# Performance work log

Measured on AMD Instinct MI355X. Metric: run time of the kernel, lower is better.

The kernel has to match this reference:

```python
import jax, jax.numpy as jnp
import numpy as np

HIDDEN = 2048
N_HEADS = 16
HEAD_DIM = HIDDEN // N_HEADS
ROPE_THETA = 10000.0
BSZ, SEQ = 2, 2048
NEG_INF = -1e9


def setup_inputs() -> dict:
    key = jax.random.key(0)
    ks = jax.random.split(key, 5)
    scale = 1.0 / np.sqrt(HIDDEN)
    hidden_states = jax.random.normal(ks[0], (BSZ, SEQ, HIDDEN), dtype=jnp.float32)
    Wq = jax.random.normal(ks[1], (HIDDEN, HIDDEN), dtype=jnp.float32) * scale
    Wk = jax.random.normal(ks[2], (HIDDEN, HIDDEN), dtype=jnp.float32) * scale
    Wv = jax.random.normal(ks[3], (HIDDEN, HIDDEN), dtype=jnp.float32) * scale
    Wo = jax.random.normal(ks[4], (HIDDEN, HIDDEN), dtype=jnp.float32) * scale
    # additive causal mask, [1, 1, S, S]
    causal = jnp.triu(jnp.full((SEQ, SEQ), NEG_INF, dtype=jnp.float32), k=1)
    attention_mask = causal[None, None, :, :]
    position_ids = jnp.arange(SEQ, dtype=jnp.int32)
    return {
        "hidden_states": hidden_states,
        "Wq": Wq, "Wk": Wk, "Wv": Wv, "Wo": Wo,
        "attention_mask": attention_mask,
        "position_ids": position_ids,
    }


def _rotate_half(x):
    half = x.shape[-1] // 2
    return jnp.concatenate((-x[..., half:], x[..., :half]), axis=-1)


def _rope_tables(seq_len, position_ids):
    # inv_freq: [head_dim/2]
    inv_freq = 1.0 / (ROPE_THETA ** (jnp.arange(0, HEAD_DIM, 2, dtype=jnp.float32) / HEAD_DIM))
    t = jnp.arange(seq_len, dtype=jnp.float32)
    freqs = t[:, None] * inv_freq[None, :]              # [S, D/2]
    emb = jnp.concatenate((freqs, freqs), axis=-1)      # [S, D]
    cos = jnp.cos(emb)[position_ids]                    # [S, D]
    sin = jnp.sin(emb)[position_ids]
    return cos, sin


def reference(hidden_states, Wq, Wk, Wv, Wo, attention_mask, position_ids):
    b, s, h = hidden_states.shape
    def proj(W):
        return (hidden_states @ W.T).reshape(b, s, N_HEADS, HEAD_DIM).transpose(0, 2, 1, 3)
    q = proj(Wq)  # [B, H, S, D]
    k = proj(Wk)
    v = proj(Wv)
    cos, sin = _rope_tables(s, position_ids)            # [S, D], broadcasts over B,H
    q = q * cos + _rotate_half(q) * sin
    k = k * cos + _rotate_half(k) * sin
    scores = jnp.einsum('bhqd,bhkd->bhqk', q, k) / np.sqrt(HEAD_DIM)
    scores = scores + attention_mask
    w = jax.nn.softmax(scores, axis=-1)
    out = jnp.einsum('bhqk,bhkd->bhqd', w, v)           # [B, H, S, D]
    out = out.transpose(0, 2, 1, 3).reshape(b, s, h)
    return out @ Wo.T
```

## Files before the change

kernel.cpp:

```cpp
#include <hip/hip_runtime.h>
#include <cstdint>
#include <cstddef>

typedef __bf16 bf16;
typedef __bf16 bf16x4 __attribute__((ext_vector_type(4)));
typedef __bf16 bf16x8 __attribute__((ext_vector_type(8)));
typedef float  f32x4  __attribute__((ext_vector_type(4)));
typedef short  s16x4  __attribute__((ext_vector_type(4)));

#define HIDDEN 2048
#define NHEADS 16
#define HDIM   128
#define BSZ    2
#define SEQ    2048
#define BS     (BSZ*SEQ)
#define QKW    (2*HIDDEN)

union b4u { bf16x4 h; s16x4 s; };

__device__ __forceinline__ void async16(const bf16* g, bf16* l) {
    __builtin_amdgcn_global_load_lds(
        (const __attribute__((address_space(1))) unsigned int*)g,
        (__attribute__((address_space(3))) unsigned int*)l, 16, 0, 0);
}

#define BARX()  asm volatile("s_barrier" ::: "memory")
#define VMW(N)  asm volatile("s_waitcnt vmcnt(" #N ")" ::: "memory")

__global__ __launch_bounds__(256) void cast_all(const float* __restrict__ hs,
                                                const float* __restrict__ Wq,
                                                const float* __restrict__ Wk,
                                                const float* __restrict__ Wv,
                                                const float* __restrict__ Wo,
                                                const int* __restrict__ pos,
                                                bf16* __restrict__ hs_b,
                                                bf16* __restrict__ wqkv,
                                                bf16* __restrict__ wo_b,
                                                float2* __restrict__ tab) {
    int i = blockIdx.x * 256 + threadIdx.x;
    if (i >= 6291456) {
        int j = i - 6291456;
        int s = j >> 6, p = j & 63;
        float t = (float)pos[s];
        float inv = expf(-(float)(2 * p) * (9.2103403719761836f / 128.0f));
        float sn, cs;
        sincosf(t * inv, &sn, &cs);
        tab[j] = make_float2(cs, sn);
        return;
    }
    const float* src; bf16* dst; int off;
    if (i < 2097152) { src = hs; dst = hs_b; off = i; }
    else {
        int j = i - 2097152;
        int r = j >> 20;
        off = j & 1048575;
        if      (r == 0) { src = Wq; dst = wqkv; }
        else if (r == 1) { src = Wk; dst = wqkv + (size_t)4194304; }
        else if (r == 2) { src = Wv; dst = wqkv + (size_t)8388608; }
        else             { src = Wo; dst = wo_b; }
    }
    const float4 v = ((const float4*)src)[off];
    bf16x4 o;
    o.x = (bf16)v.x; o.y = (bf16)v.y; o.z = (bf16)v.z; o.w = (bf16)v.w;
    ((bf16x4*)dst)[off] = o;
}

__device__ __forceinline__ int qk_perm(int n) {
    int wl = n >> 6, j = n & 63;
    return ((wl >> 1) << 7) | ((j >> 5) << 6) | ((wl & 1) << 5) | (j & 31);
}

#define QKV_TILE(T, DOSTAGE, VMN) do {                                          \
    VMW(VMN);                                                                   \
    BARX();                                                                     \
    const bf16* lAr = lA0 + ((T) & 3) * 16384;                                  \
    const bf16* lBr = lB0 + ((T) & 3) * 16384;                                  \
    bf16x8 bfr[4], af[4];                                                       \
    _Pragma("unroll") for (int nf = 0; nf < 4; ++nf)                            \
        bfr[nf] = *(const bf16x8*)(lBr + nf * 512);                             \
    _Pragma("unroll") for (int mf = 0; mf < 4; ++mf)                            \
        af[mf] = *(const bf16x8*)(lAr + mf * 512);                              \
    if (DOSTAGE) {                                                              \
        bf16* dA = smem + (((T) + 3) & 3) * 16384 + w * 512;                    \
        async16(pa0 + ((T) + 3) * 32, dA);                                      \
        async16(pa1 + ((T) + 3) * 32, dA + 4096);                               \
    }                                                                           \
    __builtin_amdgcn_s_setprio(1);                                              \
    _Pragma("unroll") for (int mf = 0; mf < 4; ++mf)                            \
    _Pragma("unroll") for (int nf = 0; nf < 4; ++nf)                            \
        acc[mf][nf] = __builtin_amdgcn_mfma_f32_16x16x32_bf16(                  \
            af[mf], bfr[nf], acc[mf][nf], 0, 0, 0);                             \
    __builtin_amdgcn_s_setprio(0);                                              \
    _Pragma("unroll") for (int mf = 0; mf < 4; ++mf)                            \
        af[mf] = *(const bf16x8*)(lAr + 2048 + mf * 512);                       \
    if (DOSTAGE) {                                                              \
        bf16* dB = smem + (((T) + 3) & 3) * 16384 + 8192 + w * 512;             \
        async16(pb0 + ((T) + 3) * 32, dB);                                      \
        async16(pb1 + ((T) + 3) * 32, dB + 4096);                               \
    }                                                                           \
    __builtin_amdgcn_s_setprio(1);                                              \
    _Pragma("unroll") for (int mf = 0; mf < 4; ++mf)                            \
    _Pragma("unroll") for (int nf = 0; nf < 4; ++nf)                            \
        acc[4 + mf][nf] = __builtin_amdgcn_mfma_f32_16x16x32_bf16(              \
            af[mf], bfr[nf], acc[4 + mf][nf], 0, 0, 0);                         \
    __builtin_amdgcn_s_setprio(0);                                              \
} while (0)

__global__ __launch_bounds__(512, 2) void gemm_qkv(const bf16* __restrict__ A,
                                                   const bf16* __restrict__ Bt,
                                                   const float2* __restrict__ tab,
                                                   bf16* __restrict__ qk,
                                                   bf16* __restrict__ vtb) {
    __shared__ alignas(16) bf16 smem[65536];

    const int tid  = threadIdx.x;
    const int lane = tid & 63;
    const int w    = tid >> 6;
    const int l15  = lane & 15;
    const int quad = lane >> 4;
    const int wm   = w >> 2;
    const int wn   = w & 3;

    const int raw = blockIdx.x;
    const int xq  = raw & 7;
    const int kq  = raw >> 3;
    const int mTile = (kq & 15) * 256;
    const int nTile = (3 * xq + (kq >> 4)) * 256;

    const int sRow  = w * 16 + (lane >> 2);
    const int sColE = ((lane & 3) * 8) ^ ((lane & 32) ? 16 : 0);
    const bf16* pa0 = A + (size_t)(mTile + sRow) * HIDDEN + sColE;
    const bf16* pa1 = pa0 + (size_t)128 * HIDDEN;
    int n0 = sRow, n1 = sRow + 128;
    if (nTile < QKW) { n0 = qk_perm(n0); n1 = qk_perm(n1); }
    const bf16* pb0 = Bt + (size_t)(nTile + n0) * HIDDEN + sColE;
    const bf16* pb1 = Bt + (size_t)(nTile + n1) * HIDDEN + sColE;

    const int colE = (quad * 8) ^ ((l15 & 8) ? 16 : 0);
    const bf16* lA0 = smem + (wm * 128 + l15) * 32 + colE;
    const bf16* lB0 = smem + 8192 + (wn * 64 + l15) * 32 + colE;

    f32x4 acc[8][4];
#pragma unroll
    for (int i = 0; i < 8; ++i)
#pragma unroll
        for (int j = 0; j < 4; ++j) acc[i][j] = (f32x4){0.f, 0.f, 0.f, 0.f};

#pragma unroll
    for (int tt = 0; tt < 3; ++tt) {
        bf16* dA = smem + tt * 16384 + w * 512;
        async16(pa0 + tt * 32, dA);
        async16(pa1 + tt * 32, dA + 4096);
        async16(pb0 + tt * 32, dA + 8192);
        async16(pb1 + tt * 32, dA + 12288);
    }

#pragma unroll 4
    for (int t = 0; t < 60; ++t) QKV_TILE(t, 1, 8);
    QKV_TILE(60, 1, 8);
    QKV_TILE(61, 0, 8);
    QKV_TILE(62, 0, 4);
    QKV_TILE(63, 0, 0);

    if (nTile < QKW) {
        const int hbase = nTile + (wn >> 1) * 128 + (wn & 1) * 32;
#pragma unroll
        for (int mf = 0; mf < 8; ++mf)
#pragma unroll
            for (int r = 0; r < 4; ++r) {
                int row = mTile + wm * 128 + mf * 16 + quad * 4 + r;
                int s   = row & (SEQ - 1);
                float2 t0 = tab[s * 64 + (wn & 1) * 32 + l15];
                float2 t1 = tab[s * 64 + (wn & 1) * 32 + 16 + l15];
                size_t rb = (size_t)row * QKW + hbase + l15;
                float lo0 = acc[mf][0][r], hi0 = acc[mf][2][r];
                float lo1 = acc[mf][1][r], hi1 = acc[mf][3][r];
                qk[rb]      = (bf16)(lo0 * t0.x - hi0 * t0.y);
                qk[rb + 64] = (bf16)(hi0 * t0.x + lo0 * t0.y);
                qk[rb + 16] = (bf16)(lo1 * t1.x - hi1 * t1.y);
                qk[rb + 80] = (bf16)(hi1 * t1.x + lo1 * t1.y);
            }
    } else {
#pragma unroll
        for (int mf = 0; mf < 8; ++mf)
#pragma unroll
            for (int nf = 0; nf < 4; ++nf) {
                int col_v = (nTile - QKW) + wn * 64 + nf * 16 + l15;
                int row0  = mTile + wm * 128 + mf * 16 + quad * 4;
                bf16x4 pk;
#pragma unroll
                for (int r = 0; r < 4; ++r) pk[r] = (bf16)acc[mf][nf][r];
                *(bf16x4*)(vtb + (size_t)col_v * BS + row0) = pk;
            }
    }
}

#define OUT_TILE(T, DOSTAGE, VMN) do {                                          \
    VMW(VMN);                                                                   \
    BARX();                                                                     \
    const bf16* lAr = lA0 + ((T) & 3) * 12288;                                  \
    const bf16* lBr = lB0 + ((T) & 3) * 12288;                                  \
    bf16x8 bfr[4], af[4];                                                       \
    _Pragma("unroll") for (int nf = 0; nf < 4; ++nf)                            \
        bfr[nf] = *(const bf16x8*)(lBr + nf * 512);                             \
    _Pragma("unroll") for (int mf = 0; mf < 4; ++mf)                            \
        af[mf] = *(const bf16x8*)(lAr + mf * 512);                              \
    if (DOSTAGE) {                                                              \
        bf16* dS = smem + (((T) + 3) & 3) * 12288 + w * 512;                    \
        async16(pa0 + ((T) + 3) * 32, dS);                                      \
        async16(pb0 + ((T) + 3) * 32, dS + 4096);                               \
        async16(pb1 + ((T) + 3) * 32, dS + 8192);                               \
    }                                                                           \
    __builtin_amdgcn_s_setprio(1);                                              \
    _Pragma("unroll") for (int mf = 0; mf < 4; ++mf)                            \
    _Pragma("unroll") for (int nf = 0; nf < 4; ++nf)                            \
        acc[mf][nf] = __builtin_amdgcn_mfma_f32_16x16x32_bf16(                  \
            af[mf], bfr[nf], acc[mf][nf], 0, 0, 0);                             \
    __builtin_amdgcn_s_setprio(0);                                              \
} while (0)

__global__ __launch_bounds__(512, 2) void gemm_out(const bf16* __restrict__ A,
                                                   const bf16* __restrict__ Bt,
                                                   float* __restrict__ C) {
    __shared__ alignas(16) bf16 smem[49152];

    const int tid  = threadIdx.x;
    const int lane = tid & 63;
    const int w    = tid >> 6;
    const int l15  = lane & 15;
    const int quad = lane >> 4;
    const int wm   = w >> 2;
    const int wn   = w & 3;

    const int raw = blockIdx.x;
    const int mTile = (raw >> 3) * 128;
    const int nTile = (raw & 7) * 256;

    const int sRow  = w * 16 + (lane >> 2);
    const int sColE = ((lane & 3) * 8) ^ ((lane & 32) ? 16 : 0);
    const bf16* pa0 = A + (size_t)(mTile + sRow) * HIDDEN + sColE;
    const bf16* pb0 = Bt + (size_t)(nTile + sRow) * HIDDEN + sColE;
    const bf16* pb1 = pb0 + (size_t)128 * HIDDEN;

    const int colE = (quad * 8) ^ ((l15 & 8) ? 16 : 0);
    const bf16* lA0 = smem + (wm * 64 + l15) * 32 + colE;
    const bf16* lB0 = smem + 4096 + (wn * 64 + l15) * 32 + colE;

    f32x4 acc[4][4];
#pragma unroll
    for (int i = 0; i < 4; ++i)
#pragma unroll
        for (int j = 0; j < 4; ++j) acc[i][j] = (f32x4){0.f, 0.f, 0.f, 0.f};

#pragma unroll
    for (int tt = 0; tt < 3; ++tt) {
        bf16* dS = smem + tt * 12288 + w * 512;
        async16(pa0 + tt * 32, dS);
        async16(pb0 + tt * 32, dS + 4096);
        async16(pb1 + tt * 32, dS + 8192);
    }

#pragma unroll 4
    for (int t = 0; t < 60; ++t) OUT_TILE(t, 1, 6);
    OUT_TILE(60, 1, 6);
    OUT_TILE(61, 0, 6);
    OUT_TILE(62, 0, 3);
    OUT_TILE(63, 0, 0);

#pragma unroll
    for (int mf = 0; mf < 4; ++mf)
#pragma unroll
        for (int nf = 0; nf < 4; ++nf)
#pragma unroll
            for (int r = 0; r < 4; ++r) {
                int row = mTile + wm * 64 + mf * 16 + quad * 4 + r;
                int col = nTile + wn * 64 + nf * 16 + l15;
                C[(size_t)row * HIDDEN + col] = acc[mf][nf][r];
            }
}

__global__ __launch_bounds__(256) void attn_kernel(const bf16* __restrict__ qk,
                                                   const bf16* __restrict__ vt,
                                                   bf16* __restrict__ ao) {
    __shared__ bf16 Kls[64 * 128];
    __shared__ bf16 Vls[128 * 64];

    const int tid  = threadIdx.x;
    const int lane = tid & 63;
    const int w    = tid >> 6;
    const int l15  = lane & 15;
    const int quad = lane >> 4;
    const int bid  = blockIdx.x;
    const int qt   = 31 - (bid >> 5);
    const int bh   = bid & 31;
    const int b    = bh >> 4;
    const int h    = bh & 15;
    const int qbase = qt * 64;
    const size_t seq0 = (size_t)b * SEQ;

    bf16x8 qf[4];
    {
        const bf16* qp = qk + (seq0 + qbase + w * 16 + l15) * QKW + h * HDIM + quad * 8;
#pragma unroll
        for (int ks = 0; ks < 4; ++ks) qf[ks] = *(const bf16x8*)(qp + ks * 32);
    }

    f32x4 o[8];
#pragma unroll
    for (int i = 0; i < 8; ++i) o[i] = (f32x4){0.f, 0.f, 0.f, 0.f};
    float m_s = -3e38f, l_s = 0.f;
    const int qg = qbase + w * 16 + l15;

    const int krow = lane >> 4;
    const int kp   = lane & 15;
    const int vrow = lane >> 3;
    const int vp   = lane & 7;
    const int sw   = l15 & 7;

    for (int t = 0; t <= qt; ++t) {
        const int kb = t * 64;
#pragma unroll
        for (int i = 0; i < 4; ++i) {
            int j = w * 16 + i * 4 + krow;
            int c = (kp & 8) | ((kp & 7) ^ (j & 7));
            async16(qk + (seq0 + kb + j) * QKW + HIDDEN + h * HDIM + c * 8,
                    Kls + (w * 4 + i) * 512);
        }
#pragma unroll
        for (int i = 0; i < 4; ++i) {
            int d = w * 32 + i * 8 + vrow;
            int c = vp ^ (d & 7);
            async16(vt + (size_t)(h * HDIM + d) * (size_t)BS + seq0 + kb + c * 8,
                    Vls + (w * 4 + i) * 512);
        }
        __syncthreads();

        f32x4 sa[4];
#pragma unroll
        for (int ni = 0; ni < 4; ++ni) sa[ni] = (f32x4){0.f, 0.f, 0.f, 0.f};
#pragma unroll
        for (int ni = 0; ni < 4; ++ni)
#pragma unroll
            for (int ks = 0; ks < 4; ++ks) {
                bf16x8 kf = *(const bf16x8*)(Kls + (ni * 16 + l15) * 128 +
                                             (((ks * 4 + quad) ^ sw) << 3));
                sa[ni] = __builtin_amdgcn_mfma_f32_16x16x32_bf16(kf, qf[ks], sa[ni], 0, 0, 0);
            }

        const float scale = 0.08838834764831845f * 1.4426950408889634f;
        float rmax = -3e38f;
        const bool diag = (t == qt);
#pragma unroll
        for (int ni = 0; ni < 4; ++ni)
#pragma unroll
            for (int r = 0; r < 4; ++r) {
                float sv = sa[ni][r] * scale;
                if (diag) {
                    int jg = kb + ni * 16 + quad * 4 + r;
                    if (jg > qg) sv = -1e30f;
                }
                sa[ni][r] = sv;
                rmax = fmaxf(rmax, sv);
            }
        rmax = fmaxf(rmax, __shfl_xor(rmax, 16));
        rmax = fmaxf(rmax, __shfl_xor(rmax, 32));

        float mn = fmaxf(m_s, rmax);
        float alpha = exp2f(m_s - mn);
        m_s = mn;
        float rsum = 0.f;
        b4u pb[4];
#pragma unroll
        for (int ni = 0; ni < 4; ++ni)
#pragma unroll
            for (int r = 0; r < 4; ++r) {
                float e = exp2f(sa[ni][r] - mn);
                rsum += e;
                pb[ni].h[r] = (bf16)e;
            }
        rsum += __shfl_xor(rsum, 16);
        rsum += __shfl_xor(rsum, 32);
        l_s = l_s * alpha + rsum;

        if (__ballot(alpha != 1.f) != 0ull) {
#pragma unroll
            for (int n2 = 0; n2 < 8; ++n2)
#pragma unroll
                for (int r = 0; r < 4; ++r) o[n2][r] *= alpha;
        }

#pragma unroll
        for (int n2 = 0; n2 < 8; ++n2)
#pragma unroll
            for (int ni = 0; ni < 4; ++ni) {
                b4u vf;
                vf.h = *(const bf16x4*)(Vls + (n2 * 16 + l15) * 64 +
                                        ((((ni * 2 + (quad >> 1)) ^ sw) << 3) + (quad & 1) * 4));
                o[n2] = __builtin_amdgcn_mfma_f32_16x16x16bf16_1k(vf.s, pb[ni].s, o[n2], 0, 0, 0);
            }
        __syncthreads();
    }

    const float inv = 1.0f / l_s;
    bf16* op = ao + (seq0 + qg) * HIDDEN + h * HDIM + quad * 4;
#pragma unroll
    for (int n2 = 0; n2 < 8; ++n2) {
        bf16x4 pk;
#pragma unroll
        for (int r = 0; r < 4; ++r) pk[r] = (bf16)(o[n2][r] * inv);
        *(bf16x4*)(op + n2 * 16) = pk;
    }
}

extern "C" void kernel_launch(void* const* d_in, const int* in_sizes, int n_in,
                              void* d_out, int out_size, void* d_ws, size_t ws_size,
                              hipStream_t stream) {
    const float* hs = (const float*)d_in[0];
    const float* Wq = (const float*)d_in[1];
    const float* Wk = (const float*)d_in[2];
    const float* Wv = (const float*)d_in[3];
    const float* Wo = (const float*)d_in[4];
    const int* pos  = (const int*)d_in[6];
    float* out = (float*)d_out;

    bf16* hs_b = (bf16*)d_ws;
    bf16* wqkv = hs_b + (size_t)8388608;
    bf16* wo_b = wqkv + (size_t)12582912;
    bf16* qkb  = wo_b + (size_t)4194304;
    bf16* vtb  = qkb + (size_t)16777216;
    bf16* ao   = vtb + (size_t)8388608;
    float2* tab = (float2*)ao;

    cast_all<<<25088, 256, 0, stream>>>(hs, Wq, Wk, Wv, Wo, pos, hs_b, wqkv, wo_b, tab);
    gemm_qkv<<<384, 512, 0, stream>>>(hs_b, wqkv, tab, qkb, vtb);
    attn_kernel<<<1024, 256, 0, stream>>>(qkb, vtb, ao);
    gemm_out<<<256, 512, 0, stream>>>(ao, wo_b, out);
}
```

Measured before the change: 371.7 us.

## Split QKV GEMM into QK and V kernels, double-buffer attention K/V

The fused QKV projection (384 blocks of 256x256 tiles) becomes two kernels. One is a 256-block QK GEMM with the RoPE epilogue. The other is a 256-block V GEMM reusing the 128x256 output-GEMM pipeline, with the shared pipeline factored into a macro. This is meant to fix wave quantization from 384 blocks and remove the per-tile branch. The attention kernel now double-buffers its K/V LDS tiles so the next tile's async load overlaps compute, with a register pin for the Q fragments. The split adds a kernel launch and re-reads hidden states, and the double buffer doubles the attention kernel's LDS use.

After: 361.8 us. 2.7% less time.

```diff
diff --git a/kernel.cpp b/kernel.cpp
--- a/kernel.cpp
+++ b/kernel.cpp
@@ -106,11 +106,10 @@
     __builtin_amdgcn_s_setprio(0);                                              \
 } while (0)
 
-__global__ __launch_bounds__(512, 2) void gemm_qkv(const bf16* __restrict__ A,
-                                                   const bf16* __restrict__ Bt,
-                                                   const float2* __restrict__ tab,
-                                                   bf16* __restrict__ qk,
-                                                   bf16* __restrict__ vtb) {
+__global__ __launch_bounds__(512, 2) void gemm_qk(const bf16* __restrict__ A,
+                                                  const bf16* __restrict__ Bt,
+                                                  const float2* __restrict__ tab,
+                                                  bf16* __restrict__ qk) {
     __shared__ alignas(16) bf16 smem[65536];
 
     const int tid  = threadIdx.x;
@@ -122,17 +121,15 @@
     const int wn   = w & 3;
 
     const int raw = blockIdx.x;
-    const int xq  = raw & 7;
     const int kq  = raw >> 3;
     const int mTile = (kq & 15) * 256;
-    const int nTile = (3 * xq + (kq >> 4)) * 256;
+    const int nTile = (2 * (raw & 7) + (kq >> 4)) * 256;
 
     const int sRow  = w * 16 + (lane >> 2);
     const int sColE = ((lane & 3) * 8) ^ ((lane & 32) ? 16 : 0);
     const bf16* pa0 = A + (size_t)(mTile + sRow) * HIDDEN + sColE;
     const bf16* pa1 = pa0 + (size_t)128 * HIDDEN;
-    int n0 = sRow, n1 = sRow + 128;
-    if (nTile < QKW) { n0 = qk_perm(n0); n1 = qk_perm(n1); }
+    const int n0 = qk_perm(sRow), n1 = qk_perm(sRow + 128);
     const bf16* pb0 = Bt + (size_t)(nTile + n0) * HIDDEN + sColE;
     const bf16* pb1 = Bt + (size_t)(nTile + n1) * HIDDEN + sColE;
 
@@ -162,37 +159,23 @@
     QKV_TILE(62, 0, 4);
     QKV_TILE(63, 0, 0);
 
-    if (nTile < QKW) {
-        const int hbase = nTile + (wn >> 1) * 128 + (wn & 1) * 32;
-#pragma unroll
-        for (int mf = 0; mf < 8; ++mf)
-#pragma unroll
-            for (int r = 0; r < 4; ++r) {
-                int row = mTile + wm * 128 + mf * 16 + quad * 4 + r;
-                int s   = row & (SEQ - 1);
-                float2 t0 = tab[s * 64 + (wn & 1) * 32 + l15];
-                float2 t1 = tab[s * 64 + (wn & 1) * 32 + 16 + l15];
-                size_t rb = (size_t)row * QKW + hbase + l15;
-                float lo0 = acc[mf][0][r], hi0 = acc[mf][2][r];
-                float lo1 = acc[mf][1][r], hi1 = acc[mf][3][r];
-                qk[rb]      = (bf16)(lo0 * t0.x - hi0 * t0.y);
-                qk[rb + 64] = (bf16)(hi0 * t0.x + lo0 * t0.y);
-                qk[rb + 16] = (bf16)(lo1 * t1.x - hi1 * t1.y);
-                qk[rb + 80] = (bf16)(hi1 * t1.x + lo1 * t1.y);
-            }
-    } else {
-#pragma unroll
-        for (int mf = 0; mf < 8; ++mf)
-#pragma unroll
-            for (int nf = 0; nf < 4; ++nf) {
-                int col_v = (nTile - QKW) + wn * 64 + nf * 16 + l15;
-                int row0  = mTile + wm * 128 + mf * 16 + quad * 4;
-                bf16x4 pk;
-#pragma unroll
-                for (int r = 0; r < 4; ++r) pk[r] = (bf16)acc[mf][nf][r];
-                *(bf16x4*)(vtb + (size_t)col_v * BS + row0) = pk;
-            }
-    }
+    const int hbase = nTile + (wn >> 1) * 128 + (wn & 1) * 32;
+#pragma unroll
+    for (int mf = 0; mf < 8; ++mf)
+#pragma unroll
+        for (int r = 0; r < 4; ++r) {
+            int row = mTile + wm * 128 + mf * 16 + quad * 4 + r;
+            int s   = row & (SEQ - 1);
+            float2 t0 = tab[s * 64 + (wn & 1) * 32 + l15];
+            float2 t1 = tab[s * 64 + (wn & 1) * 32 + 16 + l15];
+            size_t rb = (size_t)row * QKW + hbase + l15;
+            float lo0 = acc[mf][0][r], hi0 = acc[mf][2][r];
+            float lo1 = acc[mf][1][r], hi1 = acc[mf][3][r];
+            qk[rb]      = (bf16)(lo0 * t0.x - hi0 * t0.y);
+            qk[rb + 64] = (bf16)(hi0 * t0.x + lo0 * t0.y);
+            qk[rb + 16] = (bf16)(lo1 * t1.x - hi1 * t1.y);
+            qk[rb + 80] = (bf16)(hi1 * t1.x + lo1 * t1.y);
+        }
 }
 
 #define OUT_TILE(T, DOSTAGE, VMN) do {                                          \
@@ -219,54 +202,64 @@
     __builtin_amdgcn_s_setprio(0);                                              \
 } while (0)
 
+#define OUT_PROLOGUE()                                                          \
+    const int tid  = threadIdx.x;                                               \
+    const int lane = tid & 63;                                                  \
+    const int w    = tid >> 6;                                                  \
+    const int l15  = lane & 15;                                                 \
+    const int quad = lane >> 4;                                                 \
+    const int wm   = w >> 2;                                                    \
+    const int wn   = w & 3;                                                     \
+    const int raw = blockIdx.x;                                                 \
+    const int mTile = (raw >> 3) * 128;                                         \
+    const int nTile = (raw & 7) * 256;                                          \
+    const int sRow  = w * 16 + (lane >> 2);                                     \
+    const int sColE = ((lane & 3) * 8) ^ ((lane & 32) ? 16 : 0);                \
+    const bf16* pa0 = A + (size_t)(mTile + sRow) * HIDDEN + sColE;              \
+    const bf16* pb0 = Bt + (size_t)(nTile + sRow) * HIDDEN + sColE;             \
+    const bf16* pb1 = pb0 + (size_t)128 * HIDDEN;                               \
+    const int colE = (quad * 8) ^ ((l15 & 8) ? 16 : 0);                         \
+    const bf16* lA0 = smem + (wm * 64 + l15) * 32 + colE;                       \
+    const bf16* lB0 = smem + 4096 + (wn * 64 + l15) * 32 + colE;                \
+    f32x4 acc[4][4];                                                            \
+    _Pragma("unroll") for (int i = 0; i < 4; ++i)                               \
+    _Pragma("unroll") for (int j = 0; j < 4; ++j)                               \
+        acc[i][j] = (f32x4){0.f, 0.f, 0.f, 0.f};                                \
+    _Pragma("unroll") for (int tt = 0; tt < 3; ++tt) {                          \
+        bf16* dS = smem + tt * 12288 + w * 512;                                 \
+        async16(pa0 + tt * 32, dS);                                             \
+        async16(pb0 + tt * 32, dS + 4096);                                      \
+        async16(pb1 + tt * 32, dS + 8192);                                      \
+    }                                                                           \
+    _Pragma("unroll 4") for (int t = 0; t < 60; ++t) OUT_TILE(t, 1, 6);         \
+    OUT_TILE(60, 1, 6);                                                         \
+    OUT_TILE(61, 0, 6);                                                         \
+    OUT_TILE(62, 0, 3);                                                         \
+    OUT_TILE(63, 0, 0);
+
+__global__ __launch_bounds__(512, 2) void gemm_v(const bf16* __restrict__ A,
+                                                 const bf16* __restrict__ Bt,
+                                                 bf16* __restrict__ vtb) {
+    __shared__ alignas(16) bf16 smem[49152];
+    OUT_PROLOGUE()
+#pragma unroll
+    for (int mf = 0; mf < 4; ++mf)
+#pragma unroll
+        for (int nf = 0; nf < 4; ++nf) {
+            int col_v = nTile + wn * 64 + nf * 16 + l15;
+            int row0  = mTile + wm * 64 + mf * 16 + quad * 4;
+            bf16x4 pk;
+#pragma unroll
+            for (int r = 0; r < 4; ++r) pk[r] = (bf16)acc[mf][nf][r];
+            *(bf16x4*)(vtb + (size_t)col_v * BS + row0) = pk;
+        }
+}
+
 __global__ __launch_bounds__(512, 2) void gemm_out(const bf16* __restrict__ A,
                                                    const bf16* __restrict__ Bt,
                                                    float* __restrict__ C) {
     __shared__ alignas(16) bf16 smem[49152];
-
-    const int tid  = threadIdx.x;
-    const int lane = tid & 63;
-    const int w    = tid >> 6;
-    const int l15  = lane & 15;
-    const int quad = lane >> 4;
-    const int wm   = w >> 2;
-    const int wn   = w & 3;
-
-    const int raw = blockIdx.x;
-    const int mTile = (raw >> 3) * 128;
-    const int nTile = (raw & 7) * 256;
-
-    const int sRow  = w * 16 + (lane >> 2);
-    const int sColE = ((lane & 3) * 8) ^ ((lane & 32) ? 16 : 0);
-    const bf16* pa0 = A + (size_t)(mTile + sRow) * HIDDEN + sColE;
-    const bf16* pb0 = Bt + (size_t)(nTile + sRow) * HIDDEN + sColE;
-    const bf16* pb1 = pb0 + (size_t)128 * HIDDEN;
-
-    const int colE = (quad * 8) ^ ((l15 & 8) ? 16 : 0);
-    const bf16* lA0 = smem + (wm * 64 + l15) * 32 + colE;
-    const bf16* lB0 = smem + 4096 + (wn * 64 + l15) * 32 + colE;
-
-    f32x4 acc[4][4];
-#pragma unroll
-    for (int i = 0; i < 4; ++i)
-#pragma unroll
-        for (int j = 0; j < 4; ++j) acc[i][j] = (f32x4){0.f, 0.f, 0.f, 0.f};
-
-#pragma unroll
-    for (int tt = 0; tt < 3; ++tt) {
-        bf16* dS = smem + tt * 12288 + w * 512;
-        async16(pa0 + tt * 32, dS);
-        async16(pb0 + tt * 32, dS + 4096);
-        async16(pb1 + tt * 32, dS + 8192);
-    }
-
-#pragma unroll 4
-    for (int t = 0; t < 60; ++t) OUT_TILE(t, 1, 6);
-    OUT_TILE(60, 1, 6);
-    OUT_TILE(61, 0, 6);
-    OUT_TILE(62, 0, 3);
-    OUT_TILE(63, 0, 0);
-
+    OUT_PROLOGUE()
 #pragma unroll
     for (int mf = 0; mf < 4; ++mf)
 #pragma unroll
@@ -282,8 +275,8 @@
 __global__ __launch_bounds__(256) void attn_kernel(const bf16* __restrict__ qk,
                                                    const bf16* __restrict__ vt,
                                                    bf16* __restrict__ ao) {
-    __shared__ bf16 Kls[64 * 128];
-    __shared__ bf16 Vls[128 * 64];
+    __shared__ bf16 Kls[2][64 * 128];
+    __shared__ bf16 Vls[2][128 * 64];
 
     const int tid  = threadIdx.x;
     const int lane = tid & 63;
@@ -304,6 +297,9 @@
 #pragma unroll
         for (int ks = 0; ks < 4; ++ks) qf[ks] = *(const bf16x8*)(qp + ks * 32);
     }
+#pragma unroll
+    for (int ks = 0; ks < 4; ++ks)
+        asm volatile("" :: "v"(*(const f32x4*)&qf[ks]));
 
     f32x4 o[8];
 #pragma unroll
@@ -317,23 +313,31 @@
     const int vp   = lane & 7;
     const int sw   = l15 & 7;
 
+#define ATTN_STAGE(T, BUF) do {                                                  \
+        const int kb_ = (T) * 64;                                                \
+        _Pragma("unroll") for (int i = 0; i < 4; ++i) {                          \
+            int j = w * 16 + i * 4 + krow;                                       \
+            int c = (kp & 8) | ((kp & 7) ^ (j & 7));                             \
+            async16(qk + (seq0 + kb_ + j) * QKW + HIDDEN + h * HDIM + c * 8,     \
+                    &Kls[BUF][(w * 4 + i) * 512]);                               \
+        }                                                                        \
+        _Pragma("unroll") for (int i = 0; i < 4; ++i) {                          \
+            int d = w * 32 + i * 8 + vrow;                                       \
+            int c = vp ^ (d & 7);                                                \
+            async16(vt + (size_t)(h * HDIM + d) * (size_t)BS + seq0 + kb_ + c * 8,\
+                    &Vls[BUF][(w * 4 + i) * 512]);                               \
+        }                                                                        \
+    } while (0)
+
+    ATTN_STAGE(0, 0);
+
     for (int t = 0; t <= qt; ++t) {
+        if (t < qt) { ATTN_STAGE(t + 1, (t + 1) & 1); VMW(8); }
+        else        { VMW(0); }
+        BARX();
+        const bf16* Kb = Kls[t & 1];
+        const bf16* Vb = Vls[t & 1];
         const int kb = t * 64;
-#pragma unroll
-        for (int i = 0; i < 4; ++i) {
-            int j = w * 16 + i * 4 + krow;
-            int c = (kp & 8) | ((kp & 7) ^ (j & 7));
-            async16(qk + (seq0 + kb + j) * QKW + HIDDEN + h * HDIM + c * 8,
-                    Kls + (w * 4 + i) * 512);
-        }
-#pragma unroll
-        for (int i = 0; i < 4; ++i) {
-            int d = w * 32 + i * 8 + vrow;
-            int c = vp ^ (d & 7);
-            async16(vt + (size_t)(h * HDIM + d) * (size_t)BS + seq0 + kb + c * 8,
-                    Vls + (w * 4 + i) * 512);
-        }
-        __syncthreads();
 
         f32x4 sa[4];
 #pragma unroll
@@ -342,7 +346,7 @@
         for (int ni = 0; ni < 4; ++ni)
 #pragma unroll
             for (int ks = 0; ks < 4; ++ks) {
-                bf16x8 kf = *(const bf16x8*)(Kls + (ni * 16 + l15) * 128 +
+                bf16x8 kf = *(const bf16x8*)(Kb + (ni * 16 + l15) * 128 +
                                              (((ks * 4 + quad) ^ sw) << 3));
                 sa[ni] = __builtin_amdgcn_mfma_f32_16x16x32_bf16(kf, qf[ks], sa[ni], 0, 0, 0);
             }
@@ -394,12 +398,13 @@
 #pragma unroll
             for (int ni = 0; ni < 4; ++ni) {
                 b4u vf;
-                vf.h = *(const bf16x4*)(Vls + (n2 * 16 + l15) * 64 +
+                vf.h = *(const bf16x4*)(Vb + (n2 * 16 + l15) * 64 +
                                         ((((ni * 2 + (quad >> 1)) ^ sw) << 3) + (quad & 1) * 4));
                 o[n2] = __builtin_amdgcn_mfma_f32_16x16x16bf16_1k(vf.s, pb[ni].s, o[n2], 0, 0, 0);
             }
-        __syncthreads();
-    }
+        BARX();
+    }
+#undef ATTN_STAGE
 
     const float inv = 1.0f / l_s;
     bf16* op = ao + (seq0 + qg) * HIDDEN + h * HDIM + quad * 4;
@@ -432,7 +437,8 @@
     float2* tab = (float2*)ao;
 
     cast_all<<<25088, 256, 0, stream>>>(hs, Wq, Wk, Wv, Wo, pos, hs_b, wqkv, wo_b, tab);
-    gemm_qkv<<<384, 512, 0, stream>>>(hs_b, wqkv, tab, qkb, vtb);
+    gemm_qk<<<256, 512, 0, stream>>>(hs_b, wqkv, tab, qkb);
+    gemm_v<<<256, 512, 0, stream>>>(hs_b, wqkv + (size_t)8388608, vtb);
     attn_kernel<<<1024, 256, 0, stream>>>(qkb, vtb, ao);
     gemm_out<<<256, 512, 0, stream>>>(ao, wo_b, out);
 }
```
